# Performance work log

Measured on AMD Instinct MI355X. Metric: run time of the kernel, lower is better.

The kernel has to match this reference:

```python
import jax, jax.numpy as jnp
import numpy as np

# dims
N, E, C, HH, HEADS, A, V, D, AE, FH, MAXEL = 10000, 80000, 64, 128, 8, 32, 16, 64, 32, 128, 100
L, K = 2, 9  # lmax=2 -> (L+1)^2 = 9 steerable coefficients
EXPAND = jnp.array([0, 1, 1, 1, 2, 2, 2, 2, 2])          # coeff -> degree l
EXP1 = jnp.array([0, 0, 0, 1, 1, 1, 1, 1])                # coeffs 1..8 -> l-1
L_ONEHOT = jax.nn.one_hot(EXPAND, 3, dtype=jnp.float32)   # [9,3]
COUNTS = jnp.array([1 * C, 3 * C, 5 * C], dtype=jnp.float32)


def so3_linear(h, W, b):
    # per-degree linear (SO3_LinearV2): W [3,Cin,Cout], bias only on l=0
    out = jnp.einsum('nkc,kcd->nkd', h, W[EXPAND])
    return out.at[:, 0].add(b)


def enorm(h):
    # equivariant norm: per-node, per-degree RMS over (m, channels)
    sq = jnp.einsum('nkc,kl->nl', h * h, L_ONEHOT)        # [N,3] sum of squares per l
    scale = jax.lax.rsqrt(sq / COUNTS + 1e-6)             # [N,3]
    return h * scale[:, EXPAND][:, :, None]


def seg_softmax(logits, seg, n):
    m = jax.ops.segment_max(logits, seg, num_segments=n)
    m = jnp.where(jnp.isfinite(m), m, 0.0)
    e = jnp.exp(logits - m[seg])
    s = jax.ops.segment_sum(e, seg, num_segments=n)
    return e / (s[seg] + 1e-9)


def smooth_leaky_relu(z, a=0.2):
    return a * z + (1.0 - a) * z * jax.nn.sigmoid(z)


def setup_inputs():
    key = jax.random.key(0)
    ks = jax.random.split(key, 20)
    p = lambda i, sh, s=0.05: jax.random.normal(ks[i], sh, jnp.float32) * s
    return {
        'x': jax.random.normal(ks[0], (N, K, C), jnp.float32),
        'edge_distance': jax.random.uniform(ks[1], (E, D), dtype=jnp.float32),
        'rl_ij': jax.random.normal(ks[2], (E, K - 1), jnp.float32),
        'src_emb': p(3, (MAXEL, AE), 0.001),
        'tgt_emb': p(4, (MAXEL, AE), 0.001),
        'W1': p(5, (D + 2 * AE, 128)), 'b1': jnp.zeros((128,), jnp.float32),
        'W2': p(6, (128, 3 * 2 * C)), 'b2': jnp.zeros((3 * 2 * C,), jnp.float32),
        'W_conv1': p(7, (3, 2 * C, HH)),
        'W_m0': p(8, (2 * C, HEADS * A + HH + 2 * L * HH)),
        'ln_g': jnp.ones((A,), jnp.float32), 'ln_b': jnp.zeros((A,), jnp.float32),
        'alpha_dot': p(9, (HEADS, A), 0.2),
        'W_xj': p(10, (C, HH)),
        'W_conv2': p(11, (3, HH, HEADS * V)),
        'W_proj': p(12, (3, HEADS * V, C)), 'b_proj': jnp.zeros((C,), jnp.float32),
        'W_gate': p(13, (C, FH)), 'b_gate': jnp.zeros((FH,), jnp.float32),
        'W_ffn1': p(14, (3, C, FH)), 'b_ffn1': jnp.zeros((FH,), jnp.float32),
        'W_ffn2': p(15, (3, FH, C)), 'b_ffn2': jnp.zeros((C,), jnp.float32),
        'atomic_numbers': jax.random.randint(ks[16], (N,), 0, MAXEL),
        'edge_index': jax.random.randint(ks[17], (2, E), 0, N),
    }


def _block(x, edge_distance, rl_ij, src_emb, tgt_emb, W1, b1, W2, b2, W_conv1,
           W_m0, ln_g, ln_b, alpha_dot, W_xj, W_conv2, W_proj, b_proj,
           W_gate, b_gate, W_ffn1, b_ffn1, W_ffn2, b_ffn2,
           atomic_numbers, edge_index):
    src, tgt = edge_index[0], edge_index[1]
    # ---- attention branch (pre-norm) ----
    xn = enorm(x)
    xs, xt = xn[src], xn[tgt]                                    # [E,9,C] gathers
    x_edge = jnp.concatenate([xs, xt], axis=-1)                  # [E,9,2C]
    # radial function with source/target atom embeddings (use_m_share_rad)
    ef = jnp.concatenate([edge_distance, src_emb[atomic_numbers[src]],
                          tgt_emb[atomic_numbers[tgt]]], axis=-1)
    rad = jax.nn.silu(ef @ W1 + b1) @ W2 + b2                    # [E, 3*2C]
    rad = rad.reshape(E, 3, 2 * C)[:, EXPAND]                    # [E,9,2C]
    x_edge = x_edge * rad
    # so2_conv_1: per-degree linear + extra m0 scalar outputs
    msg = jnp.einsum('ekc,kcd->ekd', x_edge, W_conv1[EXPAND])    # [E,9,HH]
    extra = x_edge[:, 0] @ W_m0                                  # [E,896]
    alpha_f = extra[:, :HEADS * A].reshape(E, HEADS, A)
    g_scalar = extra[:, HEADS * A:HEADS * A + HH]                # [E,HH]
    gates = extra[:, HEADS * A + HH:].reshape(E, 2, L, HH)
    g_dir = jax.nn.sigmoid(gates[:, 0])[:, EXP1]                 # [E,8,HH]
    g_ten = jax.nn.sigmoid(gates[:, 1])[:, EXP1]                 # [E,8,HH]
    # GATA value activation: scalar silu + gated direction/tensor terms (l>=1)
    xj_proj = jnp.einsum('ekc,cd->ekd', xs, W_xj)                # [E,9,HH]
    val0 = jax.nn.silu(g_scalar)                                 # [E,HH]
    val_rest = msg[:, 1:] + rl_ij[:, :, None] * g_dir + xj_proj[:, 1:] * g_ten
    val = jnp.concatenate([val0[:, None], val_rest], axis=1)     # [E,9,HH]
    # so2_conv_2
    vout = jnp.einsum('ekd,kdh->ekh', val, W_conv2[EXPAND])      # [E,9,H*V]
    # attention weights
    mu = jnp.mean(alpha_f, axis=-1, keepdims=True)
    var = jnp.var(alpha_f, axis=-1, keepdims=True)
    an = (alpha_f - mu) * jax.lax.rsqrt(var + 1e-5) * ln_g + ln_b
    logits = jnp.einsum('eha,ha->eh', smooth_leaky_relu(an), alpha_dot)
    attn = seg_softmax(logits, tgt, N)                           # [E,HEADS]
    vout = vout.reshape(E, K, HEADS, V) * attn[:, None, :, None]
    node_out = jax.ops.segment_sum(vout.reshape(E, K, HEADS * V), tgt,
                                   num_segments=N)               # [N,9,H*V]
    x = x + so3_linear(node_out, W_proj, b_proj)
    # ---- FFN branch (pre-norm, separable S2-style gating) ----
    yn = enorm(x)
    g = yn[:, 0] @ W_gate + b_gate                               # [N,FH]
    h = so3_linear(yn, W_ffn1, b_ffn1)                           # [N,9,FH]
    h = jnp.concatenate([jax.nn.silu(g)[:, None],
                         h[:, 1:] * jax.nn.sigmoid(g)[:, None, :]], axis=1)
    return x + so3_linear(h, W_ffn2, b_ffn2)


def reference(x, edge_distance, rl_ij, src_emb, tgt_emb, W1, b1, W2, b2,
              W_conv1, W_m0, ln_g, ln_b, alpha_dot, W_xj, W_conv2, W_proj,
              b_proj, W_gate, b_gate, W_ffn1, b_ffn1, W_ffn2, b_ffn2,
              atomic_numbers, edge_index):
    return _block(x, edge_distance, rl_ij, src_emb, tgt_emb, W1, b1, W2, b2,
                  W_conv1, W_m0, ln_g, ln_b, alpha_dot, W_xj, W_conv2, W_proj,
                  b_proj, W_gate, b_gate, W_ffn1, b_ffn1, W_ffn2, b_ffn2,
                  atomic_numbers, edge_index)
```

## Files before the change

### kernel.cpp

```cpp
#include <hip/hip_runtime.h>

#define NN 10000
#define EE 80000

__device__ __forceinline__ float bf2f(unsigned short u) {
  return __uint_as_float(((unsigned)u) << 16);
}
__device__ __forceinline__ unsigned short f2bf(float f) {
  unsigned u = __float_as_uint(f);
  return (unsigned short)((u + 0x7FFFu + ((u >> 16) & 1u)) >> 16);
}
__device__ __forceinline__ float sigm(float x) { return 1.0f / (1.0f + __expf(-x)); }
__device__ __forceinline__ float siluf(float x) { return x * sigm(x); }

__device__ __forceinline__ float ld1(const void* p, long i, bool isf) {
  return isf ? ((const float*)p)[i] : bf2f(((const unsigned short*)p)[i]);
}
__device__ __forceinline__ void st1(void* p, long i, float v, bool isf) {
  if (isf) ((float*)p)[i] = v;
  else     ((unsigned short*)p)[i] = f2bf(v);
}
struct F8 { float v[8]; };
__device__ __forceinline__ F8 ld8(const void* p, long i, bool isf) {
  F8 r;
  if (isf) {
    const float* q = (const float*)p + i;
    float4 a = *(const float4*)q;
    float4 b = *(const float4*)(q + 4);
    r.v[0] = a.x; r.v[1] = a.y; r.v[2] = a.z; r.v[3] = a.w;
    r.v[4] = b.x; r.v[5] = b.y; r.v[6] = b.z; r.v[7] = b.w;
  } else {
    uint4 u = *(const uint4*)((const unsigned short*)p + i);
    r.v[0] = __uint_as_float(u.x << 16); r.v[1] = __uint_as_float(u.x & 0xFFFF0000u);
    r.v[2] = __uint_as_float(u.y << 16); r.v[3] = __uint_as_float(u.y & 0xFFFF0000u);
    r.v[4] = __uint_as_float(u.z << 16); r.v[5] = __uint_as_float(u.z & 0xFFFF0000u);
    r.v[6] = __uint_as_float(u.w << 16); r.v[7] = __uint_as_float(u.w & 0xFFFF0000u);
  }
  return r;
}

typedef __attribute__((ext_vector_type(8))) short bf8v;
typedef __attribute__((ext_vector_type(4))) float f4v;
struct AF128 { bf8v a[4]; };
struct AF64  { bf8v a[2]; };

__device__ __forceinline__ AF128 load_af128(const unsigned short* sA, int pitch, int lane) {
  AF128 f;
  const unsigned short* p = sA + (lane & 15) * pitch + ((lane >> 4) << 3);
#pragma unroll
  for (int kb = 0; kb < 4; ++kb) f.a[kb] = *(const bf8v*)(p + kb * 32);
  return f;
}
__device__ __forceinline__ AF64 load_af64(const unsigned short* sA, int pitch, int lane) {
  AF64 f;
  const unsigned short* p = sA + (lane & 15) * pitch + ((lane >> 4) << 3);
#pragma unroll
  for (int kb = 0; kb < 2; ++kb) f.a[kb] = *(const bf8v*)(p + kb * 32);
  return f;
}
__device__ __forceinline__ f4v mfma128(const AF128& f, const unsigned short* Wt,
                                       int row0, int lane) {
  const unsigned short* p = Wt + (long)(row0 + (lane & 15)) * 128 + ((lane >> 4) << 3);
  f4v acc = {0.f, 0.f, 0.f, 0.f};
#pragma unroll
  for (int kb = 0; kb < 4; ++kb)
    acc = __builtin_amdgcn_mfma_f32_16x16x32_bf16(f.a[kb], *(const bf8v*)(p + kb * 32),
                                                  acc, 0, 0, 0);
  return acc;
}
__device__ __forceinline__ f4v mfma64(const AF64& f, const unsigned short* Wt,
                                      int row0, int lane) {
  const unsigned short* p = Wt + (long)(row0 + (lane & 15)) * 64 + ((lane >> 4) << 3);
  f4v acc = {0.f, 0.f, 0.f, 0.f};
#pragma unroll
  for (int kb = 0; kb < 2; ++kb)
    acc = __builtin_amdgcn_mfma_f32_16x16x32_bf16(f.a[kb], *(const bf8v*)(p + kb * 32),
                                                  acc, 0, 0, 0);
  return acc;
}
__device__ __forceinline__ void store8(unsigned short* dst, const unsigned short v[8]) {
  uint4 u;
  u.x = (unsigned)v[0] | ((unsigned)v[1] << 16);
  u.y = (unsigned)v[2] | ((unsigned)v[3] << 16);
  u.z = (unsigned)v[4] | ((unsigned)v[5] << 16);
  u.w = (unsigned)v[6] | ((unsigned)v[7] << 16);
  *(uint4*)dst = u;
}

#define OFF_W1 0
#define OFF_W2 16384
#define OFF_M0 65536
#define OFF_C1 180224
#define OFF_XJ 229376
#define OFF_C2 237568
#define OFF_PJ 286720
#define OFF_G  311296
#define OFF_F1 319488
#define OFF_F2 344064
#define WT_TOTAL 368640

#define WS_SCALES 737280
#define WS_MBUF   857280
#define WS_SBUF   1177280
#define WS_LOGB   1497280
#define WS_CURS   2777280
#define WS_PERM   2817280
#define WS_NOUT   3137280
#define WS_XN     49217280

__global__ __launch_bounds__(256) void k_repack(
    const void* __restrict__ W1, const void* __restrict__ W2,
    const void* __restrict__ W_m0, const void* __restrict__ W_conv1,
    const void* __restrict__ W_xj, const void* __restrict__ W_conv2,
    const void* __restrict__ W_proj, const void* __restrict__ W_gate,
    const void* __restrict__ W_ffn1, const void* __restrict__ W_ffn2,
    const void* __restrict__ ln_g, unsigned short* __restrict__ wt) {
  const bool isf = (((const unsigned*)ln_g)[0] == 0x3F800000u);
  int i = blockIdx.x * 256 + threadIdx.x;
  float v;
  if (i < 16384)       { int n = i >> 7, k = i & 127; v = ld1(W1, (long)k * 128 + n, isf); }
  else if (i < 65536)  { int j = i - 16384; int n = j >> 7, k = j & 127;
                         v = ld1(W2, (long)k * 384 + n, isf); }
  else if (i < 180224) { int j = i - 65536; int n = j >> 7, k = j & 127;
                         v = ld1(W_m0, (long)k * 896 + n, isf); }
  else if (i < 229376) { int j = i - 180224; int l = j >> 14, r = j & 16383;
                         int n = r >> 7, k = r & 127;
                         v = ld1(W_conv1, (long)(l * 128 + k) * 128 + n, isf); }
  else if (i < 237568) { int j = i - 229376; int n = j >> 6, k = j & 63;
                         v = ld1(W_xj, (long)k * 128 + n, isf); }
  else if (i < 286720) { int j = i - 237568; int l = j >> 14, r = j & 16383;
                         int n = r >> 7, k = r & 127;
                         v = ld1(W_conv2, (long)(l * 128 + k) * 128 + n, isf); }
  else if (i < 311296) { int j = i - 286720; int l = j >> 13, r = j & 8191;
                         int n = r >> 7, k = r & 127;
                         v = ld1(W_proj, (long)(l * 128 + k) * 64 + n, isf); }
  else if (i < 319488) { int j = i - 311296; int n = j >> 6, k = j & 63;
                         v = ld1(W_gate, (long)k * 128 + n, isf); }
  else if (i < 344064) { int j = i - 319488; int l = j >> 13, r = j & 8191;
                         int n = r >> 6, k = r & 63;
                         v = ld1(W_ffn1, (long)(l * 64 + k) * 128 + n, isf); }
  else                 { int j = i - 344064; int l = j >> 13, r = j & 8191;
                         int n = r >> 7, k = r & 127;
                         v = ld1(W_ffn2, (long)(l * 128 + k) * 64 + n, isf); }
  wt[i] = f2bf(v);
}

__global__ __launch_bounds__(256) void k_scales(const void* __restrict__ x,
                                                const void* __restrict__ ln_g,
                                                unsigned short* __restrict__ xn) {
  const bool isf = (((const unsigned*)ln_g)[0] == 0x3F800000u);
  const int n = blockIdx.x * 4 + (threadIdx.x >> 6);
  const int c = threadIdx.x & 63;
  long xb = (long)n * 576;
  float v[9];
#pragma unroll
  for (int k = 0; k < 9; ++k) v[k] = ld1(x, xb + k * 64 + c, isf);
  float q0 = v[0] * v[0], q1 = 0.f, q2 = 0.f;
#pragma unroll
  for (int k = 1; k < 4; ++k) q1 += v[k] * v[k];
#pragma unroll
  for (int k = 4; k < 9; ++k) q2 += v[k] * v[k];
#pragma unroll
  for (int off = 32; off > 0; off >>= 1) {
    q0 += __shfl_xor(q0, off); q1 += __shfl_xor(q1, off); q2 += __shfl_xor(q2, off);
  }
  float s0 = rsqrtf(q0 * (1.f / 64.f)  + 1e-6f);
  float s1 = rsqrtf(q1 * (1.f / 192.f) + 1e-6f);
  float s2 = rsqrtf(q2 * (1.f / 320.f) + 1e-6f);
  xn[xb + c] = f2bf(v[0] * s0);
#pragma unroll
  for (int k = 1; k < 4; ++k) xn[xb + k * 64 + c] = f2bf(v[k] * s1);
#pragma unroll
  for (int k = 4; k < 9; ++k) xn[xb + k * 64 + c] = f2bf(v[k] * s2);
}

__global__ void k_init0(float* __restrict__ p) {
  int i = blockIdx.x * 256 + threadIdx.x;
  if (i < 80000) p[i] = 0.f;
}
__global__ void k_initn(float4* __restrict__ p) {
  int i = blockIdx.x * 256 + threadIdx.x;
  p[i] = make_float4(0.f, 0.f, 0.f, 0.f);
}
__global__ void k_zc(int* __restrict__ c) {
  int i = blockIdx.x * 256 + threadIdx.x;
  if (i < NN) c[i] = 0;
}
__global__ void k_hist(const int* __restrict__ edge_index, int* __restrict__ cnt) {
  int e = blockIdx.x * 256 + threadIdx.x;
  if (e < EE) atomicAdd(&cnt[edge_index[EE + e]], 1);
}
__global__ __launch_bounds__(256) void k_prefix(int* __restrict__ cur) {
  __shared__ int part[256], off0[256];
  const int th = threadIdx.x;
  int cnt[40]; int s = 0;
#pragma unroll 1
  for (int i = 0; i < 40; ++i) {
    int n = th * 40 + i;
    cnt[i] = (n < NN) ? cur[n] : 0;
    s += cnt[i];
  }
  part[th] = s;
  __syncthreads();
  if (th == 0) {
    int acc = 0;
    for (int i = 0; i < 256; ++i) { off0[i] = acc; acc += part[i]; }
  }
  __syncthreads();
  int acc = off0[th];
#pragma unroll 1
  for (int i = 0; i < 40; ++i) {
    int n = th * 40 + i;
    if (n < NN) { cur[n] = acc; acc += cnt[i]; }
  }
}
__global__ void k_scatter(const int* __restrict__ edge_index, int* __restrict__ cur,
                          int* __restrict__ perm) {
  int e = blockIdx.x * 256 + threadIdx.x;
  if (e < EE) {
    int tg = edge_index[EE + e];
    int pos = atomicAdd(&cur[tg], 1);
    perm[pos] = e;
  }
}

__global__ __launch_bounds__(256) void k_logits_e(
    const unsigned short* __restrict__ xn, const void* __restrict__ dist,
    const void* __restrict__ src_emb, const void* __restrict__ tgt_emb,
    const void* __restrict__ b1, const void* __restrict__ b2,
    const void* __restrict__ ln_g, const void* __restrict__ ln_b,
    const void* __restrict__ alpha_dot,
    const int* __restrict__ an, const int* __restrict__ edge_index,
    const unsigned short* __restrict__ wt,
    unsigned short* __restrict__ logitsb, float* __restrict__ sbuf) {
  const bool isf = (((const unsigned*)ln_g)[0] == 0x3F800000u);
  __shared__ int s_src[32], s_tgt[32], s_as[32], s_at[32];
  __shared__ __align__(16) unsigned short sA[32 * 136];
  __shared__ __align__(16) unsigned short sA2[32 * 136];
  __shared__ __align__(16) unsigned short sFB[32 * 264];

  const int t = threadIdx.x;
  const int e0 = blockIdx.x * 32;
  const int lane = t & 63, wave = t >> 6, lm = lane & 15, lq = lane >> 4;

  if (t < 32) {
    int eid = e0 + t;
    int s = edge_index[eid], g = edge_index[EE + eid];
    s_src[t] = s; s_tgt[t] = g;
    s_as[t] = an[s]; s_at[t] = an[g];
  }
  __syncthreads();
#pragma unroll
  for (int ee = 0; ee < 2; ++ee) {
    int e = ee * 16 + (t >> 4), c0 = (t & 15) * 8;
    int eid = e0 + e;
    F8 vv;
    if (c0 < 64)      vv = ld8(dist, (long)eid * 64 + c0, isf);
    else if (c0 < 96) vv = ld8(src_emb, (long)s_as[e] * 32 + (c0 - 64), isf);
    else              vv = ld8(tgt_emb, (long)s_at[e] * 32 + (c0 - 96), isf);
    unsigned short v8[8];
#pragma unroll
    for (int j = 0; j < 8; ++j) v8[j] = f2bf(vv.v[j]);
    store8(&sA[e * 136 + c0], v8);
  }
  __syncthreads();
  {
    AF128 fa0 = load_af128(sA, 136, lane);
    AF128 fa1 = load_af128(sA + 16 * 136, 136, lane);
#pragma unroll
    for (int i = 0; i < 2; ++i) {
      int nt = wave + 4 * i;
      int col = nt * 16 + lm;
      float bb = ld1(b1, col, isf);
      f4v d0 = mfma128(fa0, wt + OFF_W1, nt * 16, lane);
      f4v d1 = mfma128(fa1, wt + OFF_W1, nt * 16, lane);
#pragma unroll
      for (int r = 0; r < 4; ++r) {
        sA2[(lq * 4 + r) * 136 + col]        = f2bf(siluf(d0[r] + bb));
        sA2[(16 + lq * 4 + r) * 136 + col]   = f2bf(siluf(d1[r] + bb));
      }
    }
  }
  __syncthreads();
  {
    AF128 fh0 = load_af128(sA2, 136, lane);
    AF128 fh1 = load_af128(sA2 + 16 * 136, 136, lane);
#pragma unroll
    for (int i = 0; i < 2; ++i) {
      int nt = wave + 4 * i;
      int col = nt * 16 + lm;
      float bb = ld1(b2, col, isf);
      f4v dd[2] = { mfma128(fh0, wt + OFF_W2, nt * 16, lane),
                    mfma128(fh1, wt + OFF_W2, nt * 16, lane) };
#pragma unroll
      for (int mt = 0; mt < 2; ++mt)
#pragma unroll
        for (int r = 0; r < 4; ++r) {
          int m = mt * 16 + lq * 4 + r;
          float xv = (col < 64)
                     ? bf2f(xn[(long)s_src[m] * 576 + col])
                     : bf2f(xn[(long)s_tgt[m] * 576 + (col - 64)]);
          sA[m * 136 + col] = f2bf((dd[mt][r] + bb) * xv);
        }
    }
  }
  __syncthreads();
  {
    AF128 fe0 = load_af128(sA, 136, lane);
    AF128 fe1 = load_af128(sA + 16 * 136, 136, lane);
#pragma unroll
    for (int i = 0; i < 4; ++i) {
      int nt = wave + 4 * i;
      int col = nt * 16 + lm;
      f4v dd[2] = { mfma128(fe0, wt + OFF_M0, nt * 16, lane),
                    mfma128(fe1, wt + OFF_M0, nt * 16, lane) };
#pragma unroll
      for (int mt = 0; mt < 2; ++mt)
#pragma unroll
        for (int r = 0; r < 4; ++r)
          sFB[(mt * 16 + lq * 4 + r) * 264 + col] = f2bf(dd[mt][r]);
    }
  }
  __syncthreads();
  {
    int e = t >> 3, h = t & 7;
    const unsigned short* ap = &sFB[e * 264 + h * 32];
    float m1 = 0.f, m2 = 0.f;
#pragma unroll
    for (int a = 0; a < 32; ++a) { float v = bf2f(ap[a]); m1 += v; m2 += v * v; }
    float mu = m1 * (1.f / 32.f);
    float var = m2 * (1.f / 32.f) - mu * mu;
    float rstd = rsqrtf(fmaxf(var, 0.f) + 1e-5f);
    float acc = 0.f;
#pragma unroll
    for (int a = 0; a < 32; ++a) {
      float anv = (bf2f(ap[a]) - mu) * rstd * ld1(ln_g, a, isf) + ld1(ln_b, a, isf);
      float z = 0.2f * anv + 0.8f * anv * sigm(anv);
      acc = fmaf(z, ld1(alpha_dot, (long)h * 32 + a, isf), acc);
    }
    unsigned short lb = f2bf(acc);
    logitsb[(long)(e0 + e) * 8 + h] = lb;
    atomicAdd(&sbuf[s_tgt[e] * 8 + h], __expf(bf2f(lb)));
  }
}

__global__ __launch_bounds__(256, 4) void k_chain_e(
    const unsigned short* __restrict__ xn,
    const void* __restrict__ dist, const void* __restrict__ rl_ij,
    const void* __restrict__ src_emb, const void* __restrict__ tgt_emb,
    const void* __restrict__ b1, const void* __restrict__ b2,
    const void* __restrict__ ln_g,
    const int* __restrict__ an, const int* __restrict__ edge_index,
    const int* __restrict__ perm,
    const unsigned short* __restrict__ wt,
    const unsigned short* __restrict__ logitsb,
    const float* __restrict__ sbuf, float* __restrict__ node_out) {
  const bool isf = (((const unsigned*)ln_g)[0] == 0x3F800000u);
  __shared__ int s_src[16], s_tgt[16], s_as[16], s_at[16], s_eid[16];
  __shared__ float s_aw[16][8], s_rl[16][8];
  __shared__ __align__(16) unsigned short sPOOL[64 * 136];
  __shared__ __align__(16) unsigned short sRAD[16 * 264];
  __shared__ unsigned char sG[16 * 520];

  const int t = threadIdx.x;
  const int e0b = blockIdx.x * 16;
  const int lane = t & 63, wave = t >> 6, lm = lane & 15, lq = lane >> 4;

  if (t < 16) {
    int eid = perm[e0b + t];
    int s = edge_index[eid], g = edge_index[EE + eid];
    s_eid[t] = eid;
    s_src[t] = s; s_tgt[t] = g;
    s_as[t] = an[s]; s_at[t] = an[g];
  }
  __syncthreads();
  if (t < 128) {
    int e = t >> 3, h = t & 7;
    int eid = s_eid[e];
    float ss = sbuf[s_tgt[e] * 8 + h];
    s_aw[e][h] = __expf(bf2f(logitsb[(long)eid * 8 + h])) / (ss + 1e-9f);
    s_rl[e][h] = ld1(rl_ij, (long)eid * 8 + h, isf);
  }
  {
    int e = t >> 4, c0 = (t & 15) * 8;
    int eid = s_eid[e];
    F8 vv;
    if (c0 < 64)      vv = ld8(dist, (long)eid * 64 + c0, isf);
    else if (c0 < 96) vv = ld8(src_emb, (long)s_as[e] * 32 + (c0 - 64), isf);
    else              vv = ld8(tgt_emb, (long)s_at[e] * 32 + (c0 - 96), isf);
    unsigned short v8[8];
#pragma unroll
    for (int j = 0; j < 8; ++j) v8[j] = f2bf(vv.v[j]);
    store8(&sPOOL[e * 136 + c0], v8);
  }
  __syncthreads();
  {
    AF128 fa = load_af128(sPOOL, 136, lane);
#pragma unroll
    for (int i = 0; i < 2; ++i) {
      int nt = wave + 4 * i;
      f4v d = mfma128(fa, wt + OFF_W1, nt * 16, lane);
      int col = nt * 16 + lm;
      float bb = ld1(b1, col, isf);
#pragma unroll
      for (int r = 0; r < 4; ++r)
        sPOOL[(16 + lq * 4 + r) * 136 + col] = f2bf(siluf(d[r] + bb));
    }
  }
  __syncthreads();
  {
    AF128 fh = load_af128(sPOOL + 16 * 136, 136, lane);
#pragma unroll
    for (int i = 0; i < 6; ++i) {
      int nt = wave + 4 * i;
      f4v d = mfma128(fh, wt + OFF_W2, nt * 16, lane);
      int col = nt * 16 + lm;
      float bb = ld1(b2, col, isf);
      if (i < 2) {
#pragma unroll
        for (int r = 0; r < 4; ++r) {
          int m = lq * 4 + r;
          float xv = (col < 64)
                     ? bf2f(xn[(long)s_src[m] * 576 + col])
                     : bf2f(xn[(long)s_tgt[m] * 576 + (col - 64)]);
          sPOOL[m * 136 + col] = f2bf((d[r] + bb) * xv);
        }
      } else {
#pragma unroll
        for (int r = 0; r < 4; ++r)
          sRAD[(lq * 4 + r) * 264 + (col - 128)] = f2bf(d[r] + bb);
      }
    }
  }
  __syncthreads();
  {
    AF128 fe = load_af128(sPOOL, 136, lane);
#pragma unroll
    for (int i = 0; i < 10; ++i) {
      int nt = wave + 4 * i;
      f4v d = mfma128(fe, wt + OFF_M0 + 256 * 128, nt * 16, lane);
      int col = nt * 16 + lm;
      if (i < 2) {
#pragma unroll
        for (int r = 0; r < 4; ++r)
          sPOOL[(16 + lq * 4 + r) * 136 + col] = f2bf(siluf(d[r]));
      } else {
        int c = col - 128;
#pragma unroll
        for (int r = 0; r < 4; ++r) {
          int m = lq * 4 + r;
          unsigned char sv = (unsigned char)__float2uint_rn(sigm(d[r]) * 255.f);
          if (c < 256) sG[m * 520 + c * 2]             = sv;
          else         sG[m * 520 + (c - 256) * 2 + 1] = sv;
        }
      }
    }
  }
  __syncthreads();
  {
    AF128 fv = load_af128(sPOOL + 16 * 136, 136, lane);
#pragma unroll
    for (int i = 0; i < 2; ++i) {
      int nt = wave + 4 * i;
      f4v d = mfma128(fv, wt + OFF_C2, nt * 16, lane);
      int col = nt * 16 + lm, h = col >> 4;
      float acc = 0.f; int cur = s_tgt[lq * 4];
#pragma unroll
      for (int r = 0; r < 4; ++r) {
        int m = lq * 4 + r;
        int tg = s_tgt[m];
        float v = s_aw[m][h] * d[r];
        if (tg != cur) {
          atomicAdd(&node_out[(long)cur * 1152 + col], acc);
          acc = 0.f; cur = tg;
        }
        acc += v;
      }
      atomicAdd(&node_out[(long)cur * 1152 + col], acc);
    }
  }
  __syncthreads();

  {
    const int er = lm;
    const long sbase = (long)s_src[er] * 576 + (lq << 3);
    const long tbase = (long)s_tgt[er] * 576 + (lq << 3);
    bf8v gg[2][4];
#pragma unroll
    for (int kk = 0; kk < 2; ++kk) {
      const int k = (kk ? 5 : 1) + wave;
      gg[kk][0] = *(const bf8v*)(xn + sbase + k * 64);
      gg[kk][1] = *(const bf8v*)(xn + sbase + k * 64 + 32);
      gg[kk][2] = *(const bf8v*)(xn + tbase + k * 64);
      gg[kk][3] = *(const bf8v*)(xn + tbase + k * 64 + 32);
    }
    unsigned short* vb = sPOOL + wave * (16 * 136);
#pragma unroll
    for (int kk = 0; kk < 2; ++kk) {
      const int k = (kk ? 5 : 1) + wave;
      const int l = (k < 4) ? 1 : 2;
      const int g = l - 1;
      AF128 fm; AF64 fx;
      fx.a[0] = gg[kk][0]; fx.a[1] = gg[kk][1];
      const unsigned short* rp = sRAD + er * 264 + g * 128 + (lq << 3);
#pragma unroll
      for (int kb = 0; kb < 4; ++kb) {
        bf8v rv = *(const bf8v*)(rp + kb * 32);
        bf8v xv = gg[kk][kb];
        bf8v o;
#pragma unroll
        for (int j = 0; j < 8; ++j)
          o[j] = (short)f2bf(bf2f((unsigned short)xv[j]) *
                             bf2f((unsigned short)rv[j]));
        fm.a[kb] = o;
      }
#pragma unroll
      for (int nt = 0; nt < 8; ++nt) {
        f4v dm = mfma128(fm, wt + OFF_C1 + l * 16384, nt * 16, lane);
        f4v dx = mfma64(fx, wt + OFF_XJ, nt * 16, lane);
        int col = nt * 16 + lm;
#pragma unroll
        for (int r = 0; r < 4; ++r) {
          int m = lq * 4 + r;
          unsigned short gp =
              *(const unsigned short*)&sG[m * 520 + ((g << 7) + col) * 2];
          float gd = (float)(gp & 0xFFu) * (1.f / 255.f);
          float gt = (float)(gp >> 8)   * (1.f / 255.f);
          float val = dm[r] + s_rl[m][k - 1] * gd + dx[r] * gt;
          vb[m * 136 + col] = f2bf(val);
        }
      }
      AF128 fv = load_af128(vb, 136, lane);
#pragma unroll
      for (int nt = 0; nt < 8; ++nt) {
        f4v d = mfma128(fv, wt + OFF_C2 + l * 16384, nt * 16, lane);
        int col = nt * 16 + lm;
        float acc = 0.f; int cur = s_tgt[lq * 4];
#pragma unroll
        for (int r = 0; r < 4; ++r) {
          int m = lq * 4 + r;
          int tg = s_tgt[m];
          float v = s_aw[m][nt] * d[r];
          if (tg != cur) {
            atomicAdd(&node_out[(long)cur * 1152 + k * 128 + col], acc);
            acc = 0.f; cur = tg;
          }
          acc += v;
        }
        atomicAdd(&node_out[(long)cur * 1152 + k * 128 + col], acc);
      }
    }
  }
}

__global__ __launch_bounds__(256) void k_epi_mfma(
    const void* __restrict__ x,
    const void* __restrict__ b_proj, const void* __restrict__ b_gate,
    const void* __restrict__ b_ffn2, const void* __restrict__ ln_g,
    const unsigned short* __restrict__ wt,
    const float* __restrict__ node_out, void* __restrict__ out) {
  const bool isf = (((const unsigned*)ln_g)[0] == 0x3F800000u);
  __shared__ __align__(16) char POOL[96768];
  unsigned short* sIN = (unsigned short*)POOL;
  float* sXN = (float*)(POOL + 39168);
  unsigned short* sYN = (unsigned short*)(POOL + 76032);
  unsigned short* sH  = sIN;
  __shared__ float s_sgf[16][128];
  __shared__ float s_nsc[16][3];

  const int t = threadIdx.x;
  const int n0 = blockIdx.x * 16;
  const int lane = t & 63, wave = t >> 6, lm = lane & 15, lq = lane >> 4;

#pragma unroll
  for (int it = 0; it < 9; ++it) {
    int u = t + it * 256;
    int row = u >> 4, c0 = (u & 15) * 8;
    int k = row >> 4, n = row & 15;
    const float4* q = (const float4*)&node_out[(long)(n0 + n) * 1152 + k * 128 + c0];
    float4 a = q[0], b = q[1];
    unsigned short v8[8] = { f2bf(a.x), f2bf(a.y), f2bf(a.z), f2bf(a.w),
                             f2bf(b.x), f2bf(b.y), f2bf(b.z), f2bf(b.w) };
    store8(&sIN[row * 136 + c0], v8);
  }
  __syncthreads();
  for (int tid = wave; tid < 36; tid += 4) {
    int mt = tid >> 2, ntile = tid & 3;
    int l = (mt == 0) ? 0 : ((mt < 4) ? 1 : 2);
    AF128 fa = load_af128(sIN + mt * 16 * 136, 136, lane);
    f4v d = mfma128(fa, wt + OFF_PJ + l * 8192, ntile * 16, lane);
    int col = ntile * 16 + lm;
#pragma unroll
    for (int r = 0; r < 4; ++r) {
      int row = mt * 16 + lq * 4 + r;
      int n = row & 15, k = mt;
      float v = d[r] + ld1(x, (long)(n0 + n) * 576 + k * 64 + col, isf);
      if (k == 0) v += ld1(b_proj, col, isf);
      sXN[row * 64 + col] = v;
    }
  }
  __syncthreads();
  {
    int n = t >> 4, c4 = (t & 15) * 4;
    float q0 = 0.f, q1 = 0.f, q2 = 0.f;
#pragma unroll
    for (int k = 0; k < 9; ++k)
#pragma unroll
      for (int j = 0; j < 4; ++j) {
        float v = sXN[(k * 16 + n) * 64 + c4 + j];
        float vv = v * v;
        if (k == 0) q0 += vv; else if (k < 4) q1 += vv; else q2 += vv;
      }
#pragma unroll
    for (int off = 8; off > 0; off >>= 1) {
      q0 += __shfl_xor(q0, off); q1 += __shfl_xor(q1, off); q2 += __shfl_xor(q2, off);
    }
    if ((t & 15) == 0) {
      s_nsc[n][0] = rsqrtf(q0 * (1.f / 64.f)  + 1e-6f);
      s_nsc[n][1] = rsqrtf(q1 * (1.f / 192.f) + 1e-6f);
      s_nsc[n][2] = rsqrtf(q2 * (1.f / 320.f) + 1e-6f);
    }
  }
  __syncthreads();
#pragma unroll
  for (int it = 0; it < 5; ++it) {
    int u = t + it * 256;
    if (u < 1152) {
      int row = u >> 3, c0 = (u & 7) * 8;
      int k = row >> 4, n = row & 15;
      int l = (k == 0) ? 0 : ((k < 4) ? 1 : 2);
      float sc = s_nsc[n][l];
      unsigned short v8[8];
#pragma unroll
      for (int j = 0; j < 8; ++j) v8[j] = f2bf(sXN[row * 64 + c0 + j] * sc);
      store8(&sYN[row * 72 + c0], v8);
    }
  }
  __syncthreads();
  {
    AF64 fg = load_af64(sYN, 72, lane);
    for (int nt = wave; nt < 8; nt += 4) {
      f4v d = mfma64(fg, wt + OFF_G, nt * 16, lane);
      int col = nt * 16 + lm;
#pragma unroll
      for (int r = 0; r < 4; ++r) {
        int n = lq * 4 + r;
        float gv = d[r] + ld1(b_gate, col, isf);
        float sg = sigm(gv);
        s_sgf[n][col] = sg;
        sH[n * 136 + col] = f2bf(gv * sg);
      }
    }
  }
  __syncthreads();
  for (int tid = wave; tid < 64; tid += 4) {
    int mt = 1 + (tid >> 3), ntile = tid & 7;
    int l = (mt < 4) ? 1 : 2;
    AF64 fy = load_af64(sYN + mt * 16 * 72, 72, lane);
    f4v d = mfma64(fy, wt + OFF_F1 + l * 8192, ntile * 16, lane);
    int col = ntile * 16 + lm;
#pragma unroll
    for (int r = 0; r < 4; ++r) {
      int row = mt * 16 + lq * 4 + r;
      int n = row & 15;
      sH[row * 136 + col] = f2bf(d[r] * s_sgf[n][col]);
    }
  }
  __syncthreads();
  for (int tid = wave; tid < 36; tid += 4) {
    int mt = tid >> 2, ntile = tid & 3;
    int l = (mt == 0) ? 0 : ((mt < 4) ? 1 : 2);
    AF128 fh = load_af128(sH + mt * 16 * 136, 136, lane);
    f4v d = mfma128(fh, wt + OFF_F2 + l * 8192, ntile * 16, lane);
    int col = ntile * 16 + lm;
#pragma unroll
    for (int r = 0; r < 4; ++r) {
      int row = mt * 16 + lq * 4 + r;
      int n = row & 15, k = mt;
      float v = sXN[row * 64 + col] + d[r];
      if (k == 0) v += ld1(b_ffn2, col, isf);
      st1(out, (long)(n0 + n) * 576 + k * 64 + col, v, isf);
    }
  }
}

extern "C" void kernel_launch(void* const* d_in, const int* in_sizes, int n_in,
                              void* d_out, int out_size, void* d_ws, size_t ws_size,
                              hipStream_t stream) {
  (void)in_sizes; (void)n_in; (void)out_size; (void)ws_size;
  char* ws = (char*)d_ws;
  unsigned short* wt   = (unsigned short*)ws;
  float*    sbuf       = (float*)(ws + WS_SBUF);
  unsigned short* logb = (unsigned short*)(ws + WS_LOGB);
  int*      cursor     = (int*)(ws + WS_CURS);
  int*      perm       = (int*)(ws + WS_PERM);
  float*    node_out   = (float*)(ws + WS_NOUT);
  unsigned short* xnb  = (unsigned short*)(ws + WS_XN);
  const int* an        = (const int*)d_in[24];
  const int* ei        = (const int*)d_in[25];

  k_repack<<<WT_TOTAL / 256, 256, 0, stream>>>(
      d_in[5], d_in[7], d_in[10], d_in[9], d_in[14], d_in[15],
      d_in[16], d_in[18], d_in[20], d_in[22], d_in[11], wt);
  k_scales<<<NN / 4, 256, 0, stream>>>(d_in[0], d_in[11], xnb);
  k_init0<<<313, 256, 0, stream>>>(sbuf);
  k_initn<<<11250, 256, 0, stream>>>((float4*)node_out);
  k_zc<<<40, 256, 0, stream>>>(cursor);
  k_hist<<<(EE + 255) / 256, 256, 0, stream>>>(ei, cursor);
  k_prefix<<<1, 256, 0, stream>>>(cursor);
  k_scatter<<<(EE + 255) / 256, 256, 0, stream>>>(ei, cursor, perm);
  k_logits_e<<<EE / 32, 256, 0, stream>>>(
      xnb, d_in[1], d_in[3], d_in[4], d_in[6], d_in[8],
      d_in[11], d_in[12], d_in[13], an, ei, wt, logb, sbuf);
  k_chain_e<<<EE / 16, 256, 0, stream>>>(
      xnb, d_in[1], d_in[2], d_in[3], d_in[4], d_in[6], d_in[8], d_in[11],
      an, ei, perm, wt, logb, sbuf, node_out);
  k_epi_mfma<<<NN / 16, 256, 0, stream>>>(
      d_in[0], d_in[17], d_in[19], d_in[23], d_in[11], wt, node_out, d_out);
}
```

Measured before the change: 929.5 us.

## Pair adjacent coefficients per wave to share weight fragments in edge chain

Each wave in the edge-chain kernel now handles two adjacent steerable coefficients (kA, kB) at once instead of two strided ones. Weight B-fragments are loaded once into registers and reused across both coefficients when they share a degree, and across both M-tiles in the earlier MLP stages. The gate buffer sG is transposed so each lane reads four packed gate pairs with one 8-byte load, and the value buffer pool is doubled. The cost is higher register and LDS pressure, which lowers the occupancy hint from 4 to 3 blocks per CU.

```diff
diff --git a/kernel.cpp b/kernel.cpp
--- a/kernel.cpp
+++ b/kernel.cpp
@@ -43,6 +43,8 @@
 typedef __attribute__((ext_vector_type(4))) float f4v;
 struct AF128 { bf8v a[4]; };
 struct AF64  { bf8v a[2]; };
+struct BF128 { bf8v b[4]; };
+struct BF64  { bf8v b[2]; };
 
 __device__ __forceinline__ AF128 load_af128(const unsigned short* sA, int pitch, int lane) {
   AF128 f;
@@ -58,25 +60,41 @@
   for (int kb = 0; kb < 2; ++kb) f.a[kb] = *(const bf8v*)(p + kb * 32);
   return f;
 }
+__device__ __forceinline__ BF128 load_b128(const unsigned short* Wt, int row0, int lane) {
+  BF128 f;
+  const unsigned short* p = Wt + (long)(row0 + (lane & 15)) * 128 + ((lane >> 4) << 3);
+#pragma unroll
+  for (int kb = 0; kb < 4; ++kb) f.b[kb] = *(const bf8v*)(p + kb * 32);
+  return f;
+}
+__device__ __forceinline__ BF64 load_b64f(const unsigned short* Wt, int row0, int lane) {
+  BF64 f;
+  const unsigned short* p = Wt + (long)(row0 + (lane & 15)) * 64 + ((lane >> 4) << 3);
+#pragma unroll
+  for (int kb = 0; kb < 2; ++kb) f.b[kb] = *(const bf8v*)(p + kb * 32);
+  return f;
+}
+__device__ __forceinline__ f4v mfma128f(const AF128& a, const BF128& w) {
+  f4v acc = {0.f, 0.f, 0.f, 0.f};
+#pragma unroll
+  for (int kb = 0; kb < 4; ++kb)
+    acc = __builtin_amdgcn_mfma_f32_16x16x32_bf16(a.a[kb], w.b[kb], acc, 0, 0, 0);
+  return acc;
+}
+__device__ __forceinline__ f4v mfma64f(const AF64& a, const BF64& w) {
+  f4v acc = {0.f, 0.f, 0.f, 0.f};
+#pragma unroll
+  for (int kb = 0; kb < 2; ++kb)
+    acc = __builtin_amdgcn_mfma_f32_16x16x32_bf16(a.a[kb], w.b[kb], acc, 0, 0, 0);
+  return acc;
+}
 __device__ __forceinline__ f4v mfma128(const AF128& f, const unsigned short* Wt,
                                        int row0, int lane) {
-  const unsigned short* p = Wt + (long)(row0 + (lane & 15)) * 128 + ((lane >> 4) << 3);
-  f4v acc = {0.f, 0.f, 0.f, 0.f};
-#pragma unroll
-  for (int kb = 0; kb < 4; ++kb)
-    acc = __builtin_amdgcn_mfma_f32_16x16x32_bf16(f.a[kb], *(const bf8v*)(p + kb * 32),
-                                                  acc, 0, 0, 0);
-  return acc;
+  return mfma128f(f, load_b128(Wt, row0, lane));
 }
 __device__ __forceinline__ f4v mfma64(const AF64& f, const unsigned short* Wt,
                                       int row0, int lane) {
-  const unsigned short* p = Wt + (long)(row0 + (lane & 15)) * 64 + ((lane >> 4) << 3);
-  f4v acc = {0.f, 0.f, 0.f, 0.f};
-#pragma unroll
-  for (int kb = 0; kb < 2; ++kb)
-    acc = __builtin_amdgcn_mfma_f32_16x16x32_bf16(f.a[kb], *(const bf8v*)(p + kb * 32),
-                                                  acc, 0, 0, 0);
-  return acc;
+  return mfma64f(f, load_b64f(Wt, row0, lane));
 }
 __device__ __forceinline__ void store8(unsigned short* dst, const unsigned short v[8]) {
   uint4 u;
@@ -272,8 +290,9 @@
       int nt = wave + 4 * i;
       int col = nt * 16 + lm;
       float bb = ld1(b1, col, isf);
-      f4v d0 = mfma128(fa0, wt + OFF_W1, nt * 16, lane);
-      f4v d1 = mfma128(fa1, wt + OFF_W1, nt * 16, lane);
+      BF128 w = load_b128(wt + OFF_W1, nt * 16, lane);
+      f4v d0 = mfma128f(fa0, w);
+      f4v d1 = mfma128f(fa1, w);
 #pragma unroll
       for (int r = 0; r < 4; ++r) {
         sA2[(lq * 4 + r) * 136 + col]        = f2bf(siluf(d0[r] + bb));
@@ -290,8 +309,8 @@
       int nt = wave + 4 * i;
       int col = nt * 16 + lm;
       float bb = ld1(b2, col, isf);
-      f4v dd[2] = { mfma128(fh0, wt + OFF_W2, nt * 16, lane),
-                    mfma128(fh1, wt + OFF_W2, nt * 16, lane) };
+      BF128 w = load_b128(wt + OFF_W2, nt * 16, lane);
+      f4v dd[2] = { mfma128f(fh0, w), mfma128f(fh1, w) };
 #pragma unroll
       for (int mt = 0; mt < 2; ++mt)
 #pragma unroll
@@ -312,8 +331,8 @@
     for (int i = 0; i < 4; ++i) {
       int nt = wave + 4 * i;
       int col = nt * 16 + lm;
-      f4v dd[2] = { mfma128(fe0, wt + OFF_M0, nt * 16, lane),
-                    mfma128(fe1, wt + OFF_M0, nt * 16, lane) };
+      BF128 w = load_b128(wt + OFF_M0, nt * 16, lane);
+      f4v dd[2] = { mfma128f(fe0, w), mfma128f(fe1, w) };
 #pragma unroll
       for (int mt = 0; mt < 2; ++mt)
 #pragma unroll
@@ -344,7 +363,7 @@
   }
 }
 
-__global__ __launch_bounds__(256, 4) void k_chain_e(
+__global__ __launch_bounds__(256, 3) void k_chain_e(
     const unsigned short* __restrict__ xn,
     const void* __restrict__ dist, const void* __restrict__ rl_ij,
     const void* __restrict__ src_emb, const void* __restrict__ tgt_emb,
@@ -358,9 +377,9 @@
   const bool isf = (((const unsigned*)ln_g)[0] == 0x3F800000u);
   __shared__ int s_src[16], s_tgt[16], s_as[16], s_at[16], s_eid[16];
   __shared__ float s_aw[16][8], s_rl[16][8];
-  __shared__ __align__(16) unsigned short sPOOL[64 * 136];
+  __shared__ __align__(16) unsigned short sPOOL[128 * 136];
   __shared__ __align__(16) unsigned short sRAD[16 * 264];
-  __shared__ unsigned char sG[16 * 520];
+  __shared__ __align__(8) unsigned char sG[8192];
 
   const int t = threadIdx.x;
   const int e0b = blockIdx.x * 16;
@@ -450,8 +469,8 @@
         for (int r = 0; r < 4; ++r) {
           int m = lq * 4 + r;
           unsigned char sv = (unsigned char)__float2uint_rn(sigm(d[r]) * 255.f);
-          if (c < 256) sG[m * 520 + c * 2]             = sv;
-          else         sG[m * 520 + (c - 256) * 2 + 1] = sv;
+          if (c < 256) sG[(c << 5) + (m << 1)]             = sv;
+          else         sG[((c - 256) << 5) + (m << 1) + 1] = sv;
         }
       }
     }
@@ -482,73 +501,105 @@
   __syncthreads();
 
   {
+    const int kA = 1 + wave * 2, kB = kA + 1;
+    const int lA = (kA < 4) ? 1 : 2, lB = (kB < 4) ? 1 : 2;
+    const int gA = lA - 1, gB = lB - 1;
     const int er = lm;
     const long sbase = (long)s_src[er] * 576 + (lq << 3);
     const long tbase = (long)s_tgt[er] * 576 + (lq << 3);
-    bf8v gg[2][4];
-#pragma unroll
-    for (int kk = 0; kk < 2; ++kk) {
-      const int k = (kk ? 5 : 1) + wave;
-      gg[kk][0] = *(const bf8v*)(xn + sbase + k * 64);
-      gg[kk][1] = *(const bf8v*)(xn + sbase + k * 64 + 32);
-      gg[kk][2] = *(const bf8v*)(xn + tbase + k * 64);
-      gg[kk][3] = *(const bf8v*)(xn + tbase + k * 64 + 32);
-    }
-    unsigned short* vb = sPOOL + wave * (16 * 136);
-#pragma unroll
-    for (int kk = 0; kk < 2; ++kk) {
-      const int k = (kk ? 5 : 1) + wave;
-      const int l = (k < 4) ? 1 : 2;
-      const int g = l - 1;
-      AF128 fm; AF64 fx;
-      fx.a[0] = gg[kk][0]; fx.a[1] = gg[kk][1];
-      const unsigned short* rp = sRAD + er * 264 + g * 128 + (lq << 3);
-#pragma unroll
-      for (int kb = 0; kb < 4; ++kb) {
-        bf8v rv = *(const bf8v*)(rp + kb * 32);
-        bf8v xv = gg[kk][kb];
-        bf8v o;
-#pragma unroll
-        for (int j = 0; j < 8; ++j)
-          o[j] = (short)f2bf(bf2f((unsigned short)xv[j]) *
-                             bf2f((unsigned short)rv[j]));
-        fm.a[kb] = o;
-      }
-#pragma unroll
-      for (int nt = 0; nt < 8; ++nt) {
-        f4v dm = mfma128(fm, wt + OFF_C1 + l * 16384, nt * 16, lane);
-        f4v dx = mfma64(fx, wt + OFF_XJ, nt * 16, lane);
-        int col = nt * 16 + lm;
-#pragma unroll
-        for (int r = 0; r < 4; ++r) {
-          int m = lq * 4 + r;
-          unsigned short gp =
-              *(const unsigned short*)&sG[m * 520 + ((g << 7) + col) * 2];
-          float gd = (float)(gp & 0xFFu) * (1.f / 255.f);
-          float gt = (float)(gp >> 8)   * (1.f / 255.f);
-          float val = dm[r] + s_rl[m][k - 1] * gd + dx[r] * gt;
-          vb[m * 136 + col] = f2bf(val);
+    bf8v ggA[4], ggB[4];
+    ggA[0] = *(const bf8v*)(xn + sbase + kA * 64);
+    ggA[1] = *(const bf8v*)(xn + sbase + kA * 64 + 32);
+    ggA[2] = *(const bf8v*)(xn + tbase + kA * 64);
+    ggA[3] = *(const bf8v*)(xn + tbase + kA * 64 + 32);
+    ggB[0] = *(const bf8v*)(xn + sbase + kB * 64);
+    ggB[1] = *(const bf8v*)(xn + sbase + kB * 64 + 32);
+    ggB[2] = *(const bf8v*)(xn + tbase + kB * 64);
+    ggB[3] = *(const bf8v*)(xn + tbase + kB * 64 + 32);
+    float rlA[4], rlB[4];
+#pragma unroll
+    for (int r = 0; r < 4; ++r) {
+      rlA[r] = s_rl[lq * 4 + r][kA - 1];
+      rlB[r] = s_rl[lq * 4 + r][kB - 1];
+    }
+    AF128 fmA, fmB; AF64 fxA, fxB;
+    fxA.a[0] = ggA[0]; fxA.a[1] = ggA[1];
+    fxB.a[0] = ggB[0]; fxB.a[1] = ggB[1];
+    const unsigned short* rpA = sRAD + er * 264 + gA * 128 + (lq << 3);
+    const unsigned short* rpB = sRAD + er * 264 + gB * 128 + (lq << 3);
+#pragma unroll
+    for (int kb = 0; kb < 4; ++kb) {
+      bf8v rvA = *(const bf8v*)(rpA + kb * 32);
+      bf8v rvB = *(const bf8v*)(rpB + kb * 32);
+      bf8v oA, oB;
+#pragma unroll
+      for (int j = 0; j < 8; ++j) {
+        oA[j] = (short)f2bf(bf2f((unsigned short)ggA[kb][j]) *
+                            bf2f((unsigned short)rvA[j]));
+        oB[j] = (short)f2bf(bf2f((unsigned short)ggB[kb][j]) *
+                            bf2f((unsigned short)rvB[j]));
+      }
+      fmA.a[kb] = oA; fmB.a[kb] = oB;
+    }
+    unsigned short* vbA = sPOOL + (wave * 32) * 136;
+    unsigned short* vbB = vbA + 16 * 136;
+#pragma unroll
+    for (int nt = 0; nt < 8; ++nt) {
+      const int col = nt * 16 + lm;
+      BF128 w1A = load_b128(wt + OFF_C1 + lA * 16384, nt * 16, lane);
+      BF128 w1B;
+      if (lB == lA) w1B = w1A;
+      else          w1B = load_b128(wt + OFF_C1 + lB * 16384, nt * 16, lane);
+      BF64 wx = load_b64f(wt + OFF_XJ, nt * 16, lane);
+      f4v dmA = mfma128f(fmA, w1A);
+      f4v dmB = mfma128f(fmB, w1B);
+      f4v dxA = mfma64f(fxA, wx);
+      f4v dxB = mfma64f(fxB, wx);
+      uint2 gvA = *(const uint2*)&sG[(((gA << 7) | col) << 5) + (lq << 3)];
+      uint2 gvB;
+      if (gB == gA) gvB = gvA;
+      else          gvB = *(const uint2*)&sG[(((gB << 7) | col) << 5) + (lq << 3)];
+#pragma unroll
+      for (int r = 0; r < 4; ++r) {
+        int m = lq * 4 + r;
+        unsigned pvA = (r & 2) ? gvA.y : gvA.x;
+        unsigned ppA = (r & 1) ? (pvA >> 16) : (pvA & 0xFFFFu);
+        unsigned pvB = (r & 2) ? gvB.y : gvB.x;
+        unsigned ppB = (r & 1) ? (pvB >> 16) : (pvB & 0xFFFFu);
+        float valA = dmA[r] + rlA[r] * ((float)(ppA & 0xFFu) * (1.f / 255.f))
+                   + dxA[r] * ((float)(ppA >> 8) * (1.f / 255.f));
+        float valB = dmB[r] + rlB[r] * ((float)(ppB & 0xFFu) * (1.f / 255.f))
+                   + dxB[r] * ((float)(ppB >> 8) * (1.f / 255.f));
+        vbA[m * 136 + col] = f2bf(valA);
+        vbB[m * 136 + col] = f2bf(valB);
+      }
+    }
+    AF128 fvA = load_af128(vbA, 136, lane);
+    AF128 fvB = load_af128(vbB, 136, lane);
+#pragma unroll
+    for (int nt = 0; nt < 8; ++nt) {
+      const int col = nt * 16 + lm;
+      BF128 w2A = load_b128(wt + OFF_C2 + lA * 16384, nt * 16, lane);
+      BF128 w2B;
+      if (lB == lA) w2B = w2A;
+      else          w2B = load_b128(wt + OFF_C2 + lB * 16384, nt * 16, lane);
+      f4v dA = mfma128f(fvA, w2A);
+      f4v dB = mfma128f(fvB, w2B);
+      float accA = 0.f, accB = 0.f; int cur = s_tgt[lq * 4];
+#pragma unroll
+      for (int r = 0; r < 4; ++r) {
+        int m = lq * 4 + r;
+        int tg = s_tgt[m];
+        if (tg != cur) {
+          atomicAdd(&node_out[(long)cur * 1152 + kA * 128 + col], accA);
+          atomicAdd(&node_out[(long)cur * 1152 + kB * 128 + col], accB);
+          accA = 0.f; accB = 0.f; cur = tg;
         }
-      }
-      AF128 fv = load_af128(vb, 136, lane);
-#pragma unroll
-      for (int nt = 0; nt < 8; ++nt) {
-        f4v d = mfma128(fv, wt + OFF_C2 + l * 16384, nt * 16, lane);
-        int col = nt * 16 + lm;
-        float acc = 0.f; int cur = s_tgt[lq * 4];
-#pragma unroll
-        for (int r = 0; r < 4; ++r) {
-          int m = lq * 4 + r;
-          int tg = s_tgt[m];
-          float v = s_aw[m][nt] * d[r];
-          if (tg != cur) {
-            atomicAdd(&node_out[(long)cur * 1152 + k * 128 + col], acc);
-            acc = 0.f; cur = tg;
-          }
-          acc += v;
-        }
-        atomicAdd(&node_out[(long)cur * 1152 + k * 128 + col], acc);
-      }
+        accA += s_aw[m][nt] * dA[r];
+        accB += s_aw[m][nt] * dB[r];
+      }
+      atomicAdd(&node_out[(long)cur * 1152 + kA * 128 + col], accA);
+      atomicAdd(&node_out[(long)cur * 1152 + kB * 128 + col], accB);
     }
   }
 }
```

Result: faster. 829.1 us (-10.8%).
